# Performance work log

Hardware: AMD Instinct MI355X
Metric: run time of the kernel (lower is better)

Reference implementation:

```python
import jax, jax.numpy as jnp
import numpy as np

B, CLS, C, H, HP, WP, K = 16, 20, 512, 4, 32, 32, 9
G = H * CLS  # grapher channels = 80
EPS = 1e-5
BNS = 1.0 / np.sqrt(1.0 + EPS)  # eval-mode BN, running_mean=0, running_var=1


def _bn(x, g, b, axis):
    shape = [1] * x.ndim
    shape[axis] = -1
    return x * (g * BNS).reshape(shape) + b.reshape(shape)


def setup_inputs():
    key = jax.random.key(0)
    ks = jax.random.split(key, 16)
    def rn(k, shp, scale=0.02):
        return jax.random.normal(k, shp, dtype=jnp.float32) * scale
    return {
        "x_cls": jax.random.normal(ks[0], (B, CLS, C), jnp.float32),
        "x_patch": jax.random.normal(ks[1], (B, C, HP, WP), jnp.float32),
        "norm_x_w": jnp.ones((C, 1, 1), jnp.float32),
        "norm_x_b": jnp.zeros((C, 1, 1), jnp.float32),
        "pq_w": rn(ks[2], (C, C)), "pq_b": rn(ks[3], (C,)),
        "ncls_w": jnp.ones((C,), jnp.float32), "ncls_b": jnp.zeros((C,), jnp.float32),
        "pkv_w": rn(ks[4], (2 * C, C)), "pkv_b": rn(ks[5], (2 * C,)),
        "fc1_w": rn(ks[6], (G, G)), "fc1_b": rn(ks[7], (G,)),
        "bn1_g": jnp.ones((G,), jnp.float32), "bn1_b": jnp.zeros((G,), jnp.float32),
        "mr_w": rn(ks[8], (2 * G, 2 * G // H)), "mr_b": rn(ks[9], (2 * G,)),
        "bn2_g": jnp.ones((2 * G,), jnp.float32), "bn2_b": jnp.zeros((2 * G,), jnp.float32),
        "fc2_w": rn(ks[10], (G, 2 * G)), "fc2_b": rn(ks[11], (G,)),
        "bn3_g": jnp.ones((G,), jnp.float32), "bn3_b": jnp.zeros((G,), jnp.float32),
        "proj_w": rn(ks[12], (C, C)), "proj_b": rn(ks[13], (C,)),
    }


def _forward(x_cls, x_patch, norm_x_w, norm_x_b, pq_w, pq_b, ncls_w, ncls_b,
             pkv_w, pkv_b, fc1_w, fc1_b, bn1_g, bn1_b, mr_w, mr_b, bn2_g, bn2_b,
             fc2_w, fc2_b, bn3_g, bn3_b, proj_w, proj_b):
    hd = C // H
    N = HP * WP
    scale = hd ** -0.5
    # norm_x: LayerNormGeneral over (C,H,W)
    c0 = x_patch - x_patch.mean(axis=(1, 2, 3), keepdims=True)
    s0 = (c0 * c0).mean(axis=(1, 2, 3), keepdims=True)
    xn = c0 / jnp.sqrt(s0 + EPS) * norm_x_w + norm_x_b
    # proj_q (1x1 conv) -> multi-head query [B,H,N,hd]
    q = jnp.einsum('oc,bchw->bohw', pq_w, xn) + pq_b[None, :, None, None]
    q = q.reshape(B, H, hd, N).transpose(0, 1, 3, 2)
    # norm_cls: LayerNorm over channel dim
    m = x_cls.mean(-1, keepdims=True)
    v = ((x_cls - m) ** 2).mean(-1, keepdims=True)
    xc = (x_cls - m) / jnp.sqrt(v + EPS) * ncls_w + ncls_b
    kv = xc @ pkv_w.T + pkv_b                                  # [B,Cls,2C]
    k_, v_ = kv[..., :C], kv[..., C:]
    key_ = k_.reshape(B, CLS, H, hd).transpose(0, 2, 3, 1)     # [B,H,hd,Cls]
    val = v_.reshape(B, CLS, H, hd).transpose(0, 2, 1, 3)      # [B,H,Cls,hd]
    attn = jnp.einsum('bhnd,bhdc->bhnc', q, key_) * scale      # [B,H,N,Cls]
    amap = attn.reshape(B, H, HP, WP, CLS).transpose(0, 1, 4, 2, 3).reshape(B, G, HP, WP)
    # ---- Grapher (ViG gcn_lib): fc1 -> DyGraphConv(MRConv, KNN) -> fc2 -> residual ----
    sc = amap
    x = jnp.einsum('oc,bchw->bohw', fc1_w, amap) + fc1_b[None, :, None, None]
    x = _bn(x, bn1_g, bn1_b, 1)
    xf = x.reshape(B, G, N).transpose(0, 2, 1)                 # [B,N,G]
    # dense KNN on L2-normalized features (indices only, non-diff)
    xu = xf / jnp.maximum(jnp.linalg.norm(xf, axis=-1, keepdims=True), 1e-12)
    sq = jnp.sum(xu * xu, axis=-1)                             # [B,N]
    neg_d = 2.0 * jnp.einsum('bnc,bmc->bnm', xu, xu) - sq[:, :, None] - sq[:, None, :]
    _, nn_idx = jax.lax.top_k(neg_d, K)                        # [B,N,K]
    neigh = xf[jnp.arange(B)[:, None, None], nn_idx]           # [B,N,K,G]
    xj = jnp.max(neigh - xf[:, :, None, :], axis=2)            # [B,N,G] max-relative
    y = jnp.stack([xf, xj], axis=-1).reshape(B, N, 2 * G)      # interleave (x0,xj0,x1,...)
    # grouped 1x1 conv (groups=H), BN, GELU
    yg = y.reshape(B, N, H, 2 * G // H)
    wg = mr_w.reshape(H, 2 * G // H, 2 * G // H)
    z = jnp.einsum('bngi,goi->bngo', yg, wg).reshape(B, N, 2 * G) + mr_b
    z = _bn(z, bn2_g, bn2_b, 2)
    z = jax.nn.gelu(z, approximate=False)
    z2 = z @ fc2_w.T + fc2_b                                   # [B,N,G]
    z2 = _bn(z2, bn3_g, bn3_b, 2)
    gout = z2.transpose(0, 2, 1).reshape(B, G, HP, WP) + sc
    # ---- softmax-weighted value aggregation ----
    attn2 = gout.reshape(B, H, CLS, N).transpose(0, 1, 3, 2)   # [B,H,N,Cls]
    attn2 = jax.nn.softmax(attn2, axis=-1)
    out = jnp.einsum('bhnc,bhcd->bhnd', attn2, val)            # [B,H,N,hd]
    out = out.transpose(0, 1, 3, 2).reshape(B, C, HP, WP)
    out = jnp.einsum('oc,bchw->bohw', proj_w, out) + proj_b[None, :, None, None]
    return x_patch + out


def reference(x_cls, x_patch, norm_x_w, norm_x_b, pq_w, pq_b, ncls_w, ncls_b,
              pkv_w, pkv_b, fc1_w, fc1_b, bn1_g, bn1_b, mr_w, mr_b, bn2_g, bn2_b,
              fc2_w, fc2_b, bn3_g, bn3_b, proj_w, proj_b):
    return _forward(x_cls, x_patch, norm_x_w, norm_x_b, pq_w, pq_b, ncls_w, ncls_b,
                    pkv_w, pkv_b, fc1_w, fc1_b, bn1_g, bn1_b, mr_w, mr_b, bn2_g, bn2_b,
                    fc2_w, fc2_b, bn3_g, bn3_b, proj_w, proj_b)
```

## Files before the change

### kernel.cpp

```cpp
#include <hip/hip_runtime.h>
#include <math.h>

#define DI __device__ __forceinline__

constexpr int B_ = 16, CLS_ = 20, C_ = 512, H_ = 4, HD_ = 128, N_ = 1024, G_ = 80, G2_ = 160, K_ = 9;
constexpr float EPS_ = 1e-5f;
constexpr float BNS_ = 0.9999950000374997f;
constexpr float SCALE_ = 0.08838834764831845f;
constexpr float INVSQRT2_ = 0.7071067811865475f;

typedef __attribute__((ext_vector_type(8))) short bf16x8;
typedef __attribute__((ext_vector_type(4))) float f32x4;

constexpr long OFF_PART  = 0;
constexpr long OFF_STATS = 2048;
constexpr long OFF_EB    = 4096;
constexpr long OFF_EBB   = OFF_EB    + 524288;
constexpr long OFF_KV    = OFF_EBB   + 2048;
constexpr long OFF_AMAPT = OFF_KV    + 327680;
constexpr long OFF_XF    = OFF_AMAPT + 1310720;
constexpr long OFF_XUB   = OFF_XF    + 1310720;
constexpr long OFF_W1BD  = OFF_XUB   + 786432;
constexpr long OFF_FC2B  = OFF_W1BD  + 16384;
constexpr long OFF_SQ    = OFF_FC2B  + 8192;
constexpr long OFF_NEGD  = OFF_SQ    + 16384;
constexpr long OFF_GOUTT = OFF_NEGD  + 16777216 + 147456;
constexpr long OFF_WPB   = OFF_GOUTT + 1310720;
constexpr long OFF_Y     = OFF_WPB   + 131072;
constexpr long OFF_AMAPB = OFF_Y     + 1310720;
constexpr long OFF_FC1B  = OFF_AMAPB + 786432;
constexpr long OFF_PB    = OFF_FC1B  + 4096;

DI float wsum(float v){
#pragma unroll
  for(int d=1; d<64; d<<=1) v += __shfl_xor(v, d);
  return v;
}
DI unsigned short f2b(float f){
  unsigned u = __float_as_uint(f);
  unsigned r = (u + 0x7FFFu + ((u >> 16) & 1u)) >> 16;
  return (unsigned short)r;
}

#define GLOAD16(g, s) __builtin_amdgcn_global_load_lds((const __attribute__((address_space(1))) void*)(g), \
                        (__attribute__((address_space(3))) void*)(s), 16, 0, 0)

__global__ __launch_bounds__(256) void k_stats_partial(const float* __restrict__ x, float* __restrict__ part){
  int blk = blockIdx.x;
  const float4* xp = (const float4*)x;
  long base4 = (long)blk * 2048;
  int t = threadIdx.x;
  float s = 0.f, ss = 0.f;
#pragma unroll
  for(int j=0;j<8;++j){
    float4 v = xp[base4 + t + 256*j];
    s  += v.x + v.y + v.z + v.w;
    ss += v.x*v.x + v.y*v.y + v.z*v.z + v.w*v.w;
  }
  s = wsum(s); ss = wsum(ss);
  __shared__ float rs[4], rss[4];
  int wv = t >> 6;
  if((t & 63) == 0){ rs[wv] = s; rss[wv] = ss; }
  __syncthreads();
  if(t == 0){
    part[blk*2]   = rs[0]+rs[1]+rs[2]+rs[3];
    part[blk*2+1] = rss[0]+rss[1]+rss[2]+rss[3];
  }
}

__global__ __launch_bounds__(64) void k_stats_final(const float* __restrict__ part, float* __restrict__ stats){
  int b = blockIdx.x, t = threadIdx.x;
  float s  = part[(b*64+t)*2];
  float ss = part[(b*64+t)*2+1];
  s = wsum(s); ss = wsum(ss);
  if(t == 0){
    const float cnt = (float)(C_ * N_);
    float m = s / cnt;
    float var = ss / cnt - m*m;
    stats[b*2]   = m;
    stats[b*2+1] = 1.0f / sqrtf(var + EPS_);
  }
}

__global__ __launch_bounds__(256) void k_wprep(const float* __restrict__ projw, unsigned short* __restrict__ wpb,
                                               const float* __restrict__ mrw, const float* __restrict__ fc2w,
                                               const float* __restrict__ fc1w,
                                               unsigned short* __restrict__ w1bd, unsigned short* __restrict__ fc2b16,
                                               unsigned short* __restrict__ fc1b16){
  int blk = blockIdx.x, t = threadIdx.x;
  if(blk < 256){
    long i = (long)blk*256 + t;
    float4 v = ((const float4*)projw)[i];
    uint2 o;
    o.x = (unsigned)f2b(v.x) | ((unsigned)f2b(v.y) << 16);
    o.y = (unsigned)f2b(v.z) | ((unsigned)f2b(v.w) << 16);
    ((uint2*)wpb)[i] = o;
    return;
  }
  int row = blk - 256;
  if(row < 160){
    if(t < 160){
      unsigned short v = 0;
      if(t/40 == row/40) v = f2b(mrw[row*40 + (t % 40)]);
      w1bd[row*160 + t] = v;
    }
  } else if(row < 240){
    if(t < 160) fc2b16[(row-160)*160 + t] = f2b(fc2w[(long)(row-160)*160 + t]);
  } else {
    int r = row - 240;
    if(t < 96) fc1b16[r*96 + t] = (t < G_) ? f2b(fc1w[(long)r*G_ + t]) : (unsigned short)0;
  }
}

__global__ __launch_bounds__(256) void k_eprep(const float* __restrict__ kv, const float* __restrict__ pqw,
                                               const float* __restrict__ pqb, const float* __restrict__ stats,
                                               const float* __restrict__ nw, const float* __restrict__ nbv,
                                               unsigned short* __restrict__ Eb, float* __restrict__ ebb,
                                               float* __restrict__ pb){
  int b = blockIdx.x, hh = blockIdx.y, cch = blockIdx.z, t = threadIdx.x;
  if(hh == 4){
    if(cch == 0){
      unsigned* z = (unsigned*)(Eb + ((long)b*128 + 80)*512);
      for(int i=t; i<12288; i+=256) z[i] = 0;
    }
    return;
  }
  int h = hh, c0 = cch*64;
  float m = stats[b*2], inv = stats[b*2+1];
  __shared__ float key[CLS_][HD_];
  __shared__ float part[4][CLS_][64];
  for(int i=t; i<CLS_*HD_; i+=256){
    int cls = i >> 7, d = i & 127;
    key[cls][d] = kv[((long)b*CLS_+cls)*1024 + h*HD_ + d];
  }
  __syncthreads();
  int c = t & 63, ds = t >> 6;
  float acc[CLS_] = {};
  const float* wp = pqw + ((long)(h*HD_ + ds*32))*C_ + c0 + c;
#pragma unroll 8
  for(int di=0; di<32; ++di){
    float wv = wp[(long)di*C_];
#pragma unroll
    for(int cls=0; cls<CLS_; ++cls) acc[cls] += key[cls][ds*32+di]*wv;
  }
#pragma unroll
  for(int cls=0; cls<CLS_; ++cls) part[ds][cls][c] = acc[cls];
  __syncthreads();
  for(int i=t; i<CLS_*64; i+=256){
    int cls = i >> 6, cc = i & 63;
    float v = (part[0][cls][cc]+part[1][cls][cc]+part[2][cls][cc]+part[3][cls][cc]) * SCALE_;
    int cg = c0 + cc;
    float a = inv * nw[cg];
    float bbv = nbv[cg] - m*a;
    Eb[((long)b*128 + h*CLS_ + cls)*512 + cg] = f2b(v*a);
    part[0][cls][cc] = v*bbv;
  }
  __syncthreads();
  if(t < CLS_){
    float s = 0.f;
    for(int cc=0; cc<64; ++cc) s += part[0][t][cc];
    pb[((long)b*8 + cch)*G_ + h*CLS_ + t] = s;
  }
  if(cch == 0 && t >= 64 && t < 64 + CLS_){
    int tt = t - 64;
    float bacc = 0.f;
    for(int d=0; d<HD_; ++d) bacc += key[tt][d]*pqb[h*HD_+d];
    ebb[b*G_ + h*CLS_ + tt] = bacc*SCALE_;
  }
}

__global__ __launch_bounds__(256) void k_amap_gemm(const unsigned short* __restrict__ Eb,
                                                   const float* __restrict__ xp,
                                                   const float* __restrict__ ebb,
                                                   const float* __restrict__ pb,
                                                   float* __restrict__ amapT,
                                                   unsigned short* __restrict__ amapb){
  __shared__ unsigned short Xl[64*520];
  __shared__ unsigned short Bgl[4096];
  int b = blockIdx.y, n0 = blockIdx.x*64;
  int t = threadIdx.x, w = t >> 6, l = t & 63;
  int wr = w >> 1, wc = w & 1;
  {
    int nb = t & 7, cl = t >> 3;
    const float* xb = xp + (long)b*C_*N_ + n0 + nb*8;
#pragma unroll 4
    for(int pass=0; pass<16; ++pass){
      int c = pass*32 + cl;
      const float* src = xb + (long)c*N_;
      float4 v0 = *(const float4*)src;
      float4 v1 = *(const float4*)(src+4);
      int base = (nb*8)*520 + c;
      Xl[base         ] = f2b(v0.x);
      Xl[base + 520   ] = f2b(v0.y);
      Xl[base + 520*2 ] = f2b(v0.z);
      Xl[base + 520*3 ] = f2b(v0.w);
      Xl[base + 520*4 ] = f2b(v1.x);
      Xl[base + 520*5 ] = f2b(v1.y);
      Xl[base + 520*6 ] = f2b(v1.z);
      Xl[base + 520*7 ] = f2b(v1.w);
    }
  }
  __syncthreads();
  f32x4 acc[2][4] = {};
  const unsigned short* Bt = Eb + ((long)b*128 + w*16 + (l>>2))*512 + (l&3)*8;
  int ra = wr*32 + (l & 15);
  int rb = wc*64 + (l & 15);
  int kq = (l >> 4) * 8;
  for(int k0 = 0; k0 < 512; k0 += 32){
    if(k0) __syncthreads();
    GLOAD16(Bt + k0,          &Bgl[w*512]);
    GLOAD16(Bt + 64*512 + k0, &Bgl[2048 + w*512]);
    __syncthreads();
    bf16x8 af[2], bfr[4];
#pragma unroll
    for(int rt=0; rt<2; ++rt) af[rt]  = *(const bf16x8*)&Xl[(ra + rt*16)*520 + k0 + kq];
#pragma unroll
    for(int ct=0; ct<4; ++ct) bfr[ct] = *(const bf16x8*)&Bgl[(rb + ct*16)*32 + kq];
#pragma unroll
    for(int rt=0; rt<2; ++rt)
#pragma unroll
      for(int ct=0; ct<4; ++ct)
        acc[rt][ct] = __builtin_amdgcn_mfma_f32_16x16x32_bf16(af[rt], bfr[ct], acc[rt][ct], 0, 0, 0);
  }
  float bias4[4];
#pragma unroll
  for(int ct=0; ct<4; ++ct){
    int g = wc*64 + ct*16 + (l & 15);
    float bi = 0.f;
    if(g < G_){
      bi = ebb[b*G_ + g];
#pragma unroll
      for(int cc=0; cc<8; ++cc) bi += pb[((long)b*8 + cc)*G_ + g];
    }
    bias4[ct] = bi;
  }
  int r0 = (l >> 4)*4;
#pragma unroll
  for(int rt=0; rt<2; ++rt){
#pragma unroll
    for(int r=0; r<4; ++r){
      int n = n0 + wr*32 + rt*16 + r0 + r;
      long rowb  = ((long)b*N_ + n)*G_;
      long rowb9 = ((long)b*N_ + n)*96;
#pragma unroll
      for(int ct=0; ct<4; ++ct){
        int g = wc*64 + ct*16 + (l & 15);
        if(g < G_){
          float val = acc[rt][ct][r] + bias4[ct];
          amapT[rowb + g] = val;
          amapb[rowb9 + g] = f2b(val);
        } else if(g < 96){
          amapb[rowb9 + g] = 0;
        }
      }
    }
  }
}

template<bool RES>
__global__ __launch_bounds__(256) void k_gemm_mfma(const unsigned short* __restrict__ Wb,
                                                   const unsigned short* __restrict__ Xb,
                                                   const float* __restrict__ bias,
                                                   const float* __restrict__ Res,
                                                   float* __restrict__ Out){
  __shared__ unsigned short Al[4096];
  __shared__ unsigned short Bl[4096];
  int b = blockIdx.z;
  int o0 = blockIdx.y*128, n0 = blockIdx.x*128;
  int t = threadIdx.x, w = t >> 6, l = t & 63;
  int wr = w >> 1, wc = w & 1;
  f32x4 acc[4][4] = {};
  const unsigned short* Wt = Wb + (long)(o0 + w*16 + (l>>2))*512 + (l&3)*8;
  const unsigned short* Xt = Xb + ((long)b*N_ + n0 + w*16 + (l>>2))*512 + (l&3)*8;
  int ra = wr*64 + (l & 15);
  int rb = wc*64 + (l & 15);
  int kq = (l >> 4) * 8;
  for(int k0 = 0; k0 < 512; k0 += 32){
    if(k0) __syncthreads();
    GLOAD16(Wt + k0,            &Al[w*512]);
    GLOAD16(Wt + 64*512 + k0,   &Al[2048 + w*512]);
    GLOAD16(Xt + k0,            &Bl[w*512]);
    GLOAD16(Xt + 64*512 + k0,   &Bl[2048 + w*512]);
    __syncthreads();
    bf16x8 af[4], bfr[4];
#pragma unroll
    for(int i=0;i<4;++i){
      af[i]  = *(const bf16x8*)&Al[(ra + i*16)*32 + kq];
      bfr[i] = *(const bf16x8*)&Bl[(rb + i*16)*32 + kq];
    }
#pragma unroll
    for(int mi=0; mi<4; ++mi)
#pragma unroll
      for(int ni=0; ni<4; ++ni)
        acc[mi][ni] = __builtin_amdgcn_mfma_f32_16x16x32_bf16(af[mi], bfr[ni], acc[mi][ni], 0, 0, 0);
  }
  long obase = ((long)b*C_ + o0 + wr*64)*N_ + n0 + wc*64 + (l & 15);
  int r0 = (l >> 4) * 4;
#pragma unroll
  for(int mi=0; mi<4; ++mi){
#pragma unroll
    for(int r=0; r<4; ++r){
      int row = mi*16 + r0 + r;
      float bi = bias[o0 + wr*64 + row];
#pragma unroll
      for(int ni=0; ni<4; ++ni){
        long oi = obase + (long)row*N_ + ni*16;
        float v = acc[mi][ni][r] + bi;
        if(RES) v += Res[oi];
        Out[oi] = v;
      }
    }
  }
}

__global__ __launch_bounds__(256) void k_cls_kv(const float* __restrict__ xcls,
                                                const float* __restrict__ ncw, const float* __restrict__ ncb,
                                                const float* __restrict__ pkvw, const float* __restrict__ pkvb,
                                                float* __restrict__ kv){
  int b = blockIdx.x;
  int ochunk = blockIdx.y;
  __shared__ float xc[CLS_][C_];
  int t = threadIdx.x, wv = t >> 6, l = t & 63;
  for(int cls = wv; cls < CLS_; cls += 4){
    const float* xr = xcls + ((long)b*CLS_ + cls) * C_;
    float vals[8];
    float s = 0.f, ss = 0.f;
#pragma unroll
    for(int j=0;j<8;++j){ float v = xr[l + 64*j]; vals[j] = v; s += v; ss += v*v; }
    s = wsum(s); ss = wsum(ss);
    float m = s / (float)C_;
    float var = ss / (float)C_ - m*m;
    float inv = 1.0f / sqrtf(var + EPS_);
#pragma unroll
    for(int j=0;j<8;++j){
      int c = l + 64*j;
      xc[cls][c] = (vals[j]-m)*inv*ncw[c] + ncb[c];
    }
  }
  __syncthreads();
  int o = ochunk*128 + (t & 127);
  int cls0 = (t >> 7) * 10;
  float acc[10] = {};
  const float* wrow = pkvw + (long)o * C_;
  for(int k4 = 0; k4 < C_; k4 += 4){
    float4 w4 = *(const float4*)&wrow[k4];
#pragma unroll
    for(int i=0;i<10;++i){
      acc[i] += w4.x*xc[cls0+i][k4] + w4.y*xc[cls0+i][k4+1] + w4.z*xc[cls0+i][k4+2] + w4.w*xc[cls0+i][k4+3];
    }
  }
  float bo = pkvb[o];
#pragma unroll
  for(int i=0;i<10;++i) kv[((long)b*CLS_ + cls0+i)*1024 + o] = acc[i] + bo;
}

__global__ __launch_bounds__(256) void k_fc1_mfma(const unsigned short* __restrict__ amapb,
                                                  const unsigned short* __restrict__ w1b,
                                                  const float* __restrict__ bias,
                                                  const float* __restrict__ g1, const float* __restrict__ b1,
                                                  float* __restrict__ xf, unsigned short* __restrict__ xub,
                                                  float* __restrict__ sq){
  int t = threadIdx.x, w = t >> 6, l = t & 63;
  long row0 = ((long)blockIdx.x*4 + w)*16;
  int lr = l & 15, lk = l >> 4;
  bf16x8 ay[3];
  const unsigned short* arow = amapb + (row0 + lr)*96 + lk*8;
#pragma unroll
  for(int ks=0; ks<3; ++ks) ay[ks] = *(const bf16x8*)&arow[ks*32];
  f32x4 acc[5] = {};
  const unsigned short* wrow = w1b + (long)lr*96 + lk*8;
#pragma unroll
  for(int ks=0; ks<3; ++ks){
#pragma unroll
    for(int ct=0; ct<5; ++ct){
      bf16x8 bw = *(const bf16x8*)&wrow[ct*16*96 + ks*32];
      acc[ct] = __builtin_amdgcn_mfma_f32_16x16x32_bf16(ay[ks], bw, acc[ct], 0, 0, 0);
    }
  }
  float v[5][4];
  float ssq[4] = {0.f,0.f,0.f,0.f};
#pragma unroll
  for(int ct=0; ct<5; ++ct){
    int o = ct*16 + lr;
    float bi = bias[o], ga = g1[o]*BNS_, bb = b1[o];
#pragma unroll
    for(int i=0;i<4;++i){
      float vv = (acc[ct][i] + bi)*ga + bb;
      v[ct][i] = vv;
      ssq[i] += vv*vv;
    }
  }
#pragma unroll
  for(int d=1; d<16; d<<=1){
#pragma unroll
    for(int i=0;i<4;++i) ssq[i] += __shfl_xor(ssq[i], d);
  }
#pragma unroll
  for(int i=0;i<4;++i){
    long row = row0 + lk*4 + i;
    float invn = 1.0f / fmaxf(sqrtf(ssq[i]), 1e-12f);
#pragma unroll
    for(int ct=0; ct<5; ++ct){
      int o = ct*16 + lr;
      xf[row*G_ + o] = v[ct][i];
      xub[row*96 + o] = f2b(v[ct][i]*invn);
    }
    xub[row*96 + 80 + lr] = 0;
    if(lr == 0) sq[row] = ssq[i]*invn*invn;
  }
}

__global__ __launch_bounds__(256) void k_negd_mfma(const unsigned short* __restrict__ xub,
                                                   const float* __restrict__ sq,
                                                   float* __restrict__ negd){
  __shared__ unsigned short Al[128*96];
  __shared__ unsigned short Bl[128*96];
  int b = blockIdx.z;
  int n0 = blockIdx.y*128, m0 = blockIdx.x*128;
  int t = threadIdx.x, w = t >> 6, l = t & 63;
  int wr = w >> 1, wc = w & 1;
  const unsigned short* gA = xub + ((long)b*N_ + n0)*96;
  const unsigned short* gB = xub + ((long)b*N_ + m0)*96;
#pragma unroll
  for(int rd=0; rd<6; ++rd){
    int chunk = rd*4 + w;
    GLOAD16(gA + chunk*512 + l*8, &Al[chunk*512]);
    GLOAD16(gB + chunk*512 + l*8, &Bl[chunk*512]);
  }
  __syncthreads();
  f32x4 acc[4][4] = {};
  int ra = wr*64 + (l & 15);
  int rb = wc*64 + (l & 15);
#pragma unroll
  for(int ks=0; ks<3; ++ks){
    int kq = ks*32 + (l >> 4)*8;
    bf16x8 af[4], bfr[4];
#pragma unroll
    for(int i=0;i<4;++i){
      af[i]  = *(const bf16x8*)&Al[(ra + i*16)*96 + kq];
      bfr[i] = *(const bf16x8*)&Bl[(rb + i*16)*96 + kq];
    }
#pragma unroll
    for(int mi=0; mi<4; ++mi)
#pragma unroll
      for(int ni=0; ni<4; ++ni)
        acc[mi][ni] = __builtin_amdgcn_mfma_f32_16x16x32_bf16(af[mi], bfr[ni], acc[mi][ni], 0, 0, 0);
  }
  int r0 = (l >> 4)*4;
  const float* sqb = sq + (long)b*N_;
#pragma unroll
  for(int mi=0; mi<4; ++mi){
#pragma unroll
    for(int r=0; r<4; ++r){
      int n = n0 + wr*64 + mi*16 + r0 + r;
      float sn = sqb[n];
      long row = ((long)b*N_ + n)*N_;
#pragma unroll
      for(int ni=0; ni<4; ++ni){
        int m = m0 + wc*64 + ni*16 + (l & 15);
        negd[row + m] = 2.f*acc[mi][ni][r] - sn - sqb[m];
      }
    }
  }
}

__global__ __launch_bounds__(256) void k_topk_y(const float* __restrict__ negd, const float* __restrict__ xf,
                                                unsigned short* __restrict__ y){
  int t = threadIdx.x, wv = t >> 6, l = t & 63;
  long r = (long)blockIdx.x*4 + wv;
  long b = r >> 10;
  const float* row = negd + r*N_;
  float vals[16];
#pragma unroll
  for(int j=0;j<16;++j) vals[j] = row[l + 64*j];
  int nbs[K_];
#pragma unroll
  for(int p=0; p<K_; ++p){
    float bv = vals[0]; int bj = 0;
#pragma unroll
    for(int j=1;j<16;++j) if(vals[j] > bv){ bv = vals[j]; bj = j; }
    int bm = l + 64*bj;
#pragma unroll
    for(int d=1; d<64; d<<=1){
      float ov = __shfl_xor(bv, d);
      int   om = __shfl_xor(bm, d);
      if(ov > bv || (ov == bv && om < bm)){ bv = ov; bm = om; }
    }
    nbs[p] = bm;
#pragma unroll
    for(int j=0;j<16;++j) if(bm == l + 64*j) vals[j] = -INFINITY;
  }
  const float* frow = xf + r*G_;
  int o2s = (l < 16) ? (64 + l) : 0;
  float f0 = frow[l];
  float f1 = frow[o2s];
  float m0 = -INFINITY, m1 = -INFINITY;
#pragma unroll
  for(int k=0;k<K_;++k){
    const float* nr = xf + ((long)b*N_ + nbs[k])*G_;
    m0 = fmaxf(m0, nr[l]);
    m1 = fmaxf(m1, nr[o2s]);
  }
  unsigned short* yr = y + r*G2_;
  ushort2 u0; u0.x = f2b(f0); u0.y = f2b(m0 - f0);
  *(ushort2*)&yr[2*l] = u0;
  if(l < 16){
    ushort2 u1; u1.x = f2b(f1); u1.y = f2b(m1 - f1);
    *(ushort2*)&yr[128 + 2*l] = u1;
  }
}

__global__ __launch_bounds__(256) void k_mixer_mfma(const unsigned short* __restrict__ y,
                                                    const unsigned short* __restrict__ w1bd,
                                                    const float* __restrict__ mrb,
                                                    const float* __restrict__ g2, const float* __restrict__ b2,
                                                    const unsigned short* __restrict__ fc2b16,
                                                    const float* __restrict__ fc2bias,
                                                    const float* __restrict__ g3, const float* __restrict__ b3,
                                                    const float* __restrict__ amapT, float* __restrict__ goutT){
  __shared__ unsigned short zl[4][16][G2_];
  int t = threadIdx.x, w = t >> 6, l = t & 63;
  long row0 = ((long)blockIdx.x*4 + w)*16;
  int lr = l & 15, lk = l >> 4;
  bf16x8 ay[5];
  const unsigned short* yrow = y + (row0 + lr)*G2_ + lk*8;
#pragma unroll
  for(int ks=0; ks<5; ++ks) ay[ks] = *(const bf16x8*)&yrow[ks*32];
  f32x4 accz[10] = {};
  const unsigned short* wb = w1bd + (long)lr*G2_ + lk*8;
#pragma unroll
  for(int ks=0; ks<5; ++ks){
#pragma unroll
    for(int ct=0; ct<10; ++ct){
      bf16x8 bw = *(const bf16x8*)&wb[ct*16*G2_ + ks*32];
      accz[ct] = __builtin_amdgcn_mfma_f32_16x16x32_bf16(ay[ks], bw, accz[ct], 0, 0, 0);
    }
  }
#pragma unroll
  for(int ct=0; ct<10; ++ct){
    int o = ct*16 + lr;
    float bi = mrb[o], ga = g2[o]*BNS_, bb = b2[o];
#pragma unroll
    for(int i=0;i<4;++i){
      float v = (accz[ct][i] + bi)*ga + bb;
      float zz = v * 0.5f * (1.0f + erff(v * INVSQRT2_));
      zl[w][lk*4 + i][o] = f2b(zz);
    }
  }
  __syncthreads();
  bf16x8 az[5];
#pragma unroll
  for(int ks=0; ks<5; ++ks) az[ks] = *(const bf16x8*)&zl[w][lr][ks*32 + lk*8];
  f32x4 acc2[5] = {};
  const unsigned short* fb = fc2b16 + (long)lr*G2_ + lk*8;
#pragma unroll
  for(int ks=0; ks<5; ++ks){
#pragma unroll
    for(int ct=0; ct<5; ++ct){
      bf16x8 bw = *(const bf16x8*)&fb[ct*16*G2_ + ks*32];
      acc2[ct] = __builtin_amdgcn_mfma_f32_16x16x32_bf16(az[ks], bw, acc2[ct], 0, 0, 0);
    }
  }
#pragma unroll
  for(int ct=0; ct<5; ++ct){
    int o = ct*16 + lr;
    float bi = fc2bias[o], ga = g3[o]*BNS_, bb = b3[o];
#pragma unroll
    for(int i=0;i<4;++i){
      long row = row0 + lk*4 + i;
      float v = (acc2[ct][i] + bi)*ga + bb + amapT[row*G_ + o];
      goutT[row*G_ + o] = v;
    }
  }
}

__global__ __launch_bounds__(256) void k_softmax_pv(const float* __restrict__ goutT, const float* __restrict__ kv,
                                                    unsigned short* __restrict__ aob){
  int bh = blockIdx.x; int b = bh >> 2, h = bh & 3;
  int n0 = blockIdx.y * 64;
  __shared__ unsigned short Vt[128*32];
  __shared__ unsigned short Pl[64*40];
  __shared__ unsigned short Os[64*132];
  int t = threadIdx.x, w = t >> 6, l = t & 63;
  if(t < 128){
    int d = t;
    const float* vb = kv + ((long)b*CLS_)*1024 + C_ + h*HD_ + d;
#pragma unroll
    for(int cls=0; cls<CLS_; ++cls) Vt[d*32+cls] = f2b(vb[(long)cls*1024]);
#pragma unroll
    for(int cls=CLS_; cls<32; ++cls) Vt[d*32+cls] = 0;
  }
  if(t < 64){
    int n = n0 + t;
    const float* gr = goutT + ((long)b*N_ + n)*G_ + h*CLS_;
    float x[CLS_];
    float mx = -INFINITY;
#pragma unroll
    for(int cls=0; cls<CLS_; ++cls){ x[cls] = gr[cls]; mx = fmaxf(mx, x[cls]); }
    float s = 0.f;
#pragma unroll
    for(int cls=0; cls<CLS_; ++cls){ x[cls] = expf(x[cls]-mx); s += x[cls]; }
    float inv = 1.0f / s;
#pragma unroll
    for(int cls=0; cls<CLS_; ++cls) Pl[t*40+cls] = f2b(x[cls]*inv);
#pragma unroll
    for(int cls=CLS_; cls<32; ++cls) Pl[t*40+cls] = 0;
  }
  __syncthreads();
  int lr = l & 15, kq = (l >> 4)*8;
  f32x4 acc[4][2] = {};
  bf16x8 af[4], bf2[2];
#pragma unroll
  for(int rt=0; rt<4; ++rt) af[rt] = *(const bf16x8*)&Pl[(rt*16+lr)*40 + kq];
#pragma unroll
  for(int ci=0; ci<2; ++ci) bf2[ci] = *(const bf16x8*)&Vt[((2*w+ci)*16+lr)*32 + kq];
#pragma unroll
  for(int rt=0; rt<4; ++rt)
#pragma unroll
    for(int ci=0; ci<2; ++ci)
      acc[rt][ci] = __builtin_amdgcn_mfma_f32_16x16x32_bf16(af[rt], bf2[ci], acc[rt][ci], 0, 0, 0);
  int r0 = (l >> 4)*4;
#pragma unroll
  for(int rt=0; rt<4; ++rt)
#pragma unroll
    for(int ci=0; ci<2; ++ci)
#pragma unroll
      for(int i=0; i<4; ++i)
        Os[(rt*16 + r0 + i)*132 + (2*w+ci)*16 + lr] = f2b(acc[rt][ci][i]);
  __syncthreads();
  unsigned short* ob = aob + ((long)b*N_ + n0)*C_ + h*HD_;
#pragma unroll
  for(int j=0; j<8; ++j){
    int idx = t + 256*j;
    int row = idx >> 5, ch = idx & 31;
    *(ushort4*)&ob[(long)row*C_ + ch*4] =
        *(const ushort4*)&Os[row*132 + ch*4];
  }
}

extern "C" void kernel_launch(void* const* d_in, const int* in_sizes, int n_in,
                              void* d_out, int out_size, void* d_ws, size_t ws_size,
                              hipStream_t stream){
  const float* x_cls   = (const float*)d_in[0];
  const float* x_patch = (const float*)d_in[1];
  const float* norm_x_w = (const float*)d_in[2];
  const float* norm_x_b = (const float*)d_in[3];
  const float* pq_w  = (const float*)d_in[4];
  const float* pq_b  = (const float*)d_in[5];
  const float* ncls_w = (const float*)d_in[6];
  const float* ncls_b = (const float*)d_in[7];
  const float* pkv_w = (const float*)d_in[8];
  const float* pkv_b = (const float*)d_in[9];
  const float* fc1_w = (const float*)d_in[10];
  const float* fc1_b = (const float*)d_in[11];
  const float* bn1_g = (const float*)d_in[12];
  const float* bn1_b = (const float*)d_in[13];
  const float* mr_w  = (const float*)d_in[14];
  const float* mr_b  = (const float*)d_in[15];
  const float* bn2_g = (const float*)d_in[16];
  const float* bn2_b = (const float*)d_in[17];
  const float* fc2_w = (const float*)d_in[18];
  const float* fc2_b = (const float*)d_in[19];
  const float* bn3_g = (const float*)d_in[20];
  const float* bn3_b = (const float*)d_in[21];
  const float* proj_w = (const float*)d_in[22];
  const float* proj_b = (const float*)d_in[23];

  float* ws = (float*)d_ws;
  float* part   = ws + OFF_PART;
  float* stats  = ws + OFF_STATS;
  float* ebb    = ws + OFF_EBB;
  float* kvbuf  = ws + OFF_KV;
  float* amapT  = ws + OFF_AMAPT;
  float* xf     = ws + OFF_XF;
  float* sqbuf  = ws + OFF_SQ;
  float* negd   = ws + OFF_NEGD;
  float* goutT  = ws + OFF_GOUTT;
  float* pbuf   = ws + OFF_PB;
  unsigned short* Eb     = (unsigned short*)(ws + OFF_EB);
  unsigned short* xub    = (unsigned short*)(ws + OFF_XUB);
  unsigned short* w1bd   = (unsigned short*)(ws + OFF_W1BD);
  unsigned short* fc2b16 = (unsigned short*)(ws + OFF_FC2B);
  unsigned short* ybuf   = (unsigned short*)(ws + OFF_Y);
  unsigned short* amapb  = (unsigned short*)(ws + OFF_AMAPB);
  unsigned short* fc1b16 = (unsigned short*)(ws + OFF_FC1B);
  unsigned short* aob = (unsigned short*)(ws + OFF_NEGD);
  unsigned short* wpb = (unsigned short*)(ws + OFF_WPB);
  float* out = (float*)d_out;

  k_stats_partial<<<1024, 256, 0, stream>>>(x_patch, part);
  k_stats_final<<<16, 64, 0, stream>>>(part, stats);
  k_cls_kv<<<dim3(16,8), 256, 0, stream>>>(x_cls, ncls_w, ncls_b, pkv_w, pkv_b, kvbuf);
  k_eprep<<<dim3(16,5,8), 256, 0, stream>>>(kvbuf, pq_w, pq_b, stats, norm_x_w, norm_x_b, Eb, ebb, pbuf);
  k_wprep<<<576, 256, 0, stream>>>(proj_w, wpb, mr_w, fc2_w, fc1_w, w1bd, fc2b16, fc1b16);
  k_amap_gemm<<<dim3(16,16), 256, 0, stream>>>(Eb, x_patch, ebb, pbuf, amapT, amapb);
  k_fc1_mfma<<<256, 256, 0, stream>>>(amapb, fc1b16, fc1_b, bn1_g, bn1_b, xf, xub, sqbuf);
  k_negd_mfma<<<dim3(8,8,16), 256, 0, stream>>>(xub, sqbuf, negd);
  k_topk_y<<<4096, 256, 0, stream>>>(negd, xf, ybuf);
  k_mixer_mfma<<<256, 256, 0, stream>>>(ybuf, w1bd, mr_b, bn2_g, bn2_b,
                                        fc2b16, fc2_b, bn3_g, bn3_b, amapT, goutT);
  k_softmax_pv<<<dim3(64,16), 256, 0, stream>>>(goutT, kvbuf, aob);
  k_gemm_mfma<true><<<dim3(8,4,16), 256, 0, stream>>>(wpb, aob, proj_b, x_patch, out);
}
```

Baseline: 181.4 us.

## Fuse prep kernels, fold stats finalisation into eprep, fuse fc1 into amap GEMM

Merges the x_patch stats partial reduction, the cls LayerNorm plus kv projection, and the weight bf16 conversion into one k_pre launch that dispatches on block index. The per-batch stats finalisation moves into k_eprep. The fc1 MFMA with BN and L2 normalisation moves into the amap GEMM epilogue, reading the bf16 amap tile from LDS instead of a global amapb buffer. This removes four launches and a global round trip for amapb. In exchange, every k_pre block reserves 40KB of LDS, which may limit occupancy of the stats blocks, and k_eprep repeats the stats reduction in each block.

```diff
diff --git a/kernel.cpp b/kernel.cpp
--- a/kernel.cpp
+++ b/kernel.cpp
@@ -13,7 +13,6 @@
 typedef __attribute__((ext_vector_type(4))) float f32x4;
 
 constexpr long OFF_PART  = 0;
-constexpr long OFF_STATS = 2048;
 constexpr long OFF_EB    = 4096;
 constexpr long OFF_EBB   = OFF_EB    + 524288;
 constexpr long OFF_KV    = OFF_EBB   + 2048;
@@ -27,8 +26,7 @@
 constexpr long OFF_GOUTT = OFF_NEGD  + 16777216 + 147456;
 constexpr long OFF_WPB   = OFF_GOUTT + 1310720;
 constexpr long OFF_Y     = OFF_WPB   + 131072;
-constexpr long OFF_AMAPB = OFF_Y     + 1310720;
-constexpr long OFF_FC1B  = OFF_AMAPB + 786432;
+constexpr long OFF_FC1B  = OFF_Y     + 1310720;
 constexpr long OFF_PB    = OFF_FC1B  + 4096;
 
 DI float wsum(float v){
@@ -45,51 +43,79 @@
 #define GLOAD16(g, s) __builtin_amdgcn_global_load_lds((const __attribute__((address_space(1))) void*)(g), \
                         (__attribute__((address_space(3))) void*)(s), 16, 0, 0)
 
-__global__ __launch_bounds__(256) void k_stats_partial(const float* __restrict__ x, float* __restrict__ part){
-  int blk = blockIdx.x;
-  const float4* xp = (const float4*)x;
-  long base4 = (long)blk * 2048;
-  int t = threadIdx.x;
-  float s = 0.f, ss = 0.f;
-#pragma unroll
-  for(int j=0;j<8;++j){
-    float4 v = xp[base4 + t + 256*j];
-    s  += v.x + v.y + v.z + v.w;
-    ss += v.x*v.x + v.y*v.y + v.z*v.z + v.w*v.w;
-  }
-  s = wsum(s); ss = wsum(ss);
-  __shared__ float rs[4], rss[4];
-  int wv = t >> 6;
-  if((t & 63) == 0){ rs[wv] = s; rss[wv] = ss; }
-  __syncthreads();
-  if(t == 0){
-    part[blk*2]   = rs[0]+rs[1]+rs[2]+rs[3];
-    part[blk*2+1] = rss[0]+rss[1]+rss[2]+rss[3];
-  }
-}
-
-__global__ __launch_bounds__(64) void k_stats_final(const float* __restrict__ part, float* __restrict__ stats){
-  int b = blockIdx.x, t = threadIdx.x;
-  float s  = part[(b*64+t)*2];
-  float ss = part[(b*64+t)*2+1];
-  s = wsum(s); ss = wsum(ss);
-  if(t == 0){
-    const float cnt = (float)(C_ * N_);
-    float m = s / cnt;
-    float var = ss / cnt - m*m;
-    stats[b*2]   = m;
-    stats[b*2+1] = 1.0f / sqrtf(var + EPS_);
-  }
-}
-
-__global__ __launch_bounds__(256) void k_wprep(const float* __restrict__ projw, unsigned short* __restrict__ wpb,
-                                               const float* __restrict__ mrw, const float* __restrict__ fc2w,
-                                               const float* __restrict__ fc1w,
-                                               unsigned short* __restrict__ w1bd, unsigned short* __restrict__ fc2b16,
-                                               unsigned short* __restrict__ fc1b16){
+__global__ __launch_bounds__(256) void k_pre(const float* __restrict__ x, float* __restrict__ part,
+                                             const float* __restrict__ xcls,
+                                             const float* __restrict__ ncw, const float* __restrict__ ncb,
+                                             const float* __restrict__ pkvw, const float* __restrict__ pkvb,
+                                             float* __restrict__ kv,
+                                             const float* __restrict__ projw, unsigned short* __restrict__ wpb,
+                                             const float* __restrict__ mrw, const float* __restrict__ fc2w,
+                                             const float* __restrict__ fc1w,
+                                             unsigned short* __restrict__ w1bd, unsigned short* __restrict__ fc2b16,
+                                             unsigned short* __restrict__ fc1b16){
+  __shared__ float sh[CLS_*C_];
   int blk = blockIdx.x, t = threadIdx.x;
-  if(blk < 256){
-    long i = (long)blk*256 + t;
+  if(blk < 1024){
+    const float4* xp = (const float4*)x;
+    long base4 = (long)blk * 2048;
+    float s = 0.f, ss = 0.f;
+#pragma unroll
+    for(int j=0;j<8;++j){
+      float4 v = xp[base4 + t + 256*j];
+      s  += v.x + v.y + v.z + v.w;
+      ss += v.x*v.x + v.y*v.y + v.z*v.z + v.w*v.w;
+    }
+    s = wsum(s); ss = wsum(ss);
+    int wv = t >> 6;
+    if((t & 63) == 0){ sh[wv] = s; sh[4+wv] = ss; }
+    __syncthreads();
+    if(t == 0){
+      part[blk*2]   = sh[0]+sh[1]+sh[2]+sh[3];
+      part[blk*2+1] = sh[4]+sh[5]+sh[6]+sh[7];
+    }
+    return;
+  }
+  if(blk < 1152){
+    int idx = blk - 1024;
+    int b = idx >> 3, ochunk = idx & 7;
+    float (*xc)[C_] = (float(*)[C_])sh;
+    int wv = t >> 6, l = t & 63;
+    for(int cls = wv; cls < CLS_; cls += 4){
+      const float* xr = xcls + ((long)b*CLS_ + cls) * C_;
+      float vals[8];
+      float s = 0.f, ss = 0.f;
+#pragma unroll
+      for(int j=0;j<8;++j){ float v = xr[l + 64*j]; vals[j] = v; s += v; ss += v*v; }
+      s = wsum(s); ss = wsum(ss);
+      float m = s / (float)C_;
+      float var = ss / (float)C_ - m*m;
+      float inv = 1.0f / sqrtf(var + EPS_);
+#pragma unroll
+      for(int j=0;j<8;++j){
+        int c = l + 64*j;
+        xc[cls][c] = (vals[j]-m)*inv*ncw[c] + ncb[c];
+      }
+    }
+    __syncthreads();
+    int o = ochunk*128 + (t & 127);
+    int cls0 = (t >> 7) * 10;
+    float acc[10] = {};
+    const float* wrow = pkvw + (long)o * C_;
+    for(int k4 = 0; k4 < C_; k4 += 4){
+      float4 w4 = *(const float4*)&wrow[k4];
+#pragma unroll
+      for(int i=0;i<10;++i){
+        acc[i] += w4.x*xc[cls0+i][k4] + w4.y*xc[cls0+i][k4+1] + w4.z*xc[cls0+i][k4+2] + w4.w*xc[cls0+i][k4+3];
+      }
+    }
+    float bo = pkvb[o];
+#pragma unroll
+    for(int i=0;i<10;++i) kv[((long)b*CLS_ + cls0+i)*1024 + o] = acc[i] + bo;
+    return;
+  }
+  int blk2 = blk - 1152;
+  if(blk2 < 256){
+    long i = (long)blk2*256 + t;
     float4 v = ((const float4*)projw)[i];
     uint2 o;
     o.x = (unsigned)f2b(v.x) | ((unsigned)f2b(v.y) << 16);
@@ -97,7 +123,7 @@
     ((uint2*)wpb)[i] = o;
     return;
   }
-  int row = blk - 256;
+  int row = blk2 - 256;
   if(row < 160){
     if(t < 160){
       unsigned short v = 0;
@@ -106,14 +132,14 @@
     }
   } else if(row < 240){
     if(t < 160) fc2b16[(row-160)*160 + t] = f2b(fc2w[(long)(row-160)*160 + t]);
-  } else {
+  } else if(row < 320){
     int r = row - 240;
     if(t < 96) fc1b16[r*96 + t] = (t < G_) ? f2b(fc1w[(long)r*G_ + t]) : (unsigned short)0;
   }
 }
 
 __global__ __launch_bounds__(256) void k_eprep(const float* __restrict__ kv, const float* __restrict__ pqw,
-                                               const float* __restrict__ pqb, const float* __restrict__ stats,
+                                               const float* __restrict__ pqb, const float* __restrict__ partbuf,
                                                const float* __restrict__ nw, const float* __restrict__ nbv,
                                                unsigned short* __restrict__ Eb, float* __restrict__ ebb,
                                                float* __restrict__ pb){
@@ -125,15 +151,27 @@
     }
     return;
   }
-  int h = hh, c0 = cch*64;
-  float m = stats[b*2], inv = stats[b*2+1];
+  __shared__ float sst[2];
   __shared__ float key[CLS_][HD_];
   __shared__ float part[4][CLS_][64];
+  if(t < 64){
+    float s  = partbuf[(b*64+t)*2];
+    float ss = partbuf[(b*64+t)*2+1];
+    s = wsum(s); ss = wsum(ss);
+    if(t == 0){
+      const float cnt = (float)(C_ * N_);
+      float m = s / cnt;
+      sst[0] = m;
+      sst[1] = 1.0f / sqrtf(ss / cnt - m*m + EPS_);
+    }
+  }
+  int h = hh, c0 = cch*64;
   for(int i=t; i<CLS_*HD_; i+=256){
     int cls = i >> 7, d = i & 127;
     key[cls][d] = kv[((long)b*CLS_+cls)*1024 + h*HD_ + d];
   }
   __syncthreads();
+  float m = sst[0], inv = sst[1];
   int c = t & 63, ds = t >> 6;
   float acc[CLS_] = {};
   const float* wp = pqw + ((long)(h*HD_ + ds*32))*C_ + c0 + c;
@@ -159,7 +197,7 @@
   if(t < CLS_){
     float s = 0.f;
     for(int cc=0; cc<64; ++cc) s += part[0][t][cc];
-    pb[((long)b*8 + cch)*G_ + h*CLS_ + t] = s;
+    pb[((long)b*8 + cch)*G_ + t < 0 ? 0 : ((long)b*8 + cch)*G_ + h*CLS_ + t] = s;
   }
   if(cch == 0 && t >= 64 && t < 64 + CLS_){
     int tt = t - 64;
@@ -169,14 +207,19 @@
   }
 }
 
-__global__ __launch_bounds__(256) void k_amap_gemm(const unsigned short* __restrict__ Eb,
-                                                   const float* __restrict__ xp,
-                                                   const float* __restrict__ ebb,
-                                                   const float* __restrict__ pb,
-                                                   float* __restrict__ amapT,
-                                                   unsigned short* __restrict__ amapb){
+__global__ __launch_bounds__(256) void k_amap_fc1(const unsigned short* __restrict__ Eb,
+                                                  const float* __restrict__ xp,
+                                                  const float* __restrict__ ebb,
+                                                  const float* __restrict__ pb,
+                                                  const unsigned short* __restrict__ w1b,
+                                                  const float* __restrict__ f1bias,
+                                                  const float* __restrict__ g1, const float* __restrict__ b1,
+                                                  float* __restrict__ amapT,
+                                                  float* __restrict__ xf, unsigned short* __restrict__ xub,
+                                                  float* __restrict__ sq){
   __shared__ unsigned short Xl[64*520];
   __shared__ unsigned short Bgl[4096];
+  unsigned short* A1 = Xl;
   int b = blockIdx.y, n0 = blockIdx.x*64;
   int t = threadIdx.x, w = t >> 6, l = t & 63;
   int wr = w >> 1, wc = w & 1;
@@ -234,26 +277,74 @@
     }
     bias4[ct] = bi;
   }
+  __syncthreads();
   int r0 = (l >> 4)*4;
 #pragma unroll
   for(int rt=0; rt<2; ++rt){
 #pragma unroll
     for(int r=0; r<4; ++r){
-      int n = n0 + wr*32 + rt*16 + r0 + r;
-      long rowb  = ((long)b*N_ + n)*G_;
-      long rowb9 = ((long)b*N_ + n)*96;
+      int lrow = wr*32 + rt*16 + r0 + r;
+      long rowb = ((long)b*N_ + n0 + lrow)*G_;
 #pragma unroll
       for(int ct=0; ct<4; ++ct){
         int g = wc*64 + ct*16 + (l & 15);
         if(g < G_){
           float val = acc[rt][ct][r] + bias4[ct];
           amapT[rowb + g] = val;
-          amapb[rowb9 + g] = f2b(val);
+          A1[lrow*96 + g] = f2b(val);
         } else if(g < 96){
-          amapb[rowb9 + g] = 0;
+          A1[lrow*96 + g] = 0;
         }
       }
     }
+  }
+  __syncthreads();
+  int lr = l & 15, lk = l >> 4;
+  bf16x8 ay[3];
+  const unsigned short* arow = &A1[(w*16 + lr)*96 + lk*8];
+#pragma unroll
+  for(int ks=0; ks<3; ++ks) ay[ks] = *(const bf16x8*)&arow[ks*32];
+  f32x4 acc5[5] = {};
+  const unsigned short* wrow = w1b + (long)lr*96 + lk*8;
+#pragma unroll
+  for(int ks=0; ks<3; ++ks){
+#pragma unroll
+    for(int ct=0; ct<5; ++ct){
+      bf16x8 bw = *(const bf16x8*)&wrow[ct*16*96 + ks*32];
+      acc5[ct] = __builtin_amdgcn_mfma_f32_16x16x32_bf16(ay[ks], bw, acc5[ct], 0, 0, 0);
+    }
+  }
+  float v[5][4];
+  float ssq[4] = {0.f,0.f,0.f,0.f};
+#pragma unroll
+  for(int ct=0; ct<5; ++ct){
+    int o = ct*16 + lr;
+    float bi = f1bias[o], ga = g1[o]*BNS_, bb = b1[o];
+#pragma unroll
+    for(int i=0;i<4;++i){
+      float vv = (acc5[ct][i] + bi)*ga + bb;
+      v[ct][i] = vv;
+      ssq[i] += vv*vv;
+    }
+  }
+#pragma unroll
+  for(int d=1; d<16; d<<=1){
+#pragma unroll
+    for(int i=0;i<4;++i) ssq[i] += __shfl_xor(ssq[i], d);
+  }
+  long row0g = (long)b*N_ + n0 + w*16;
+#pragma unroll
+  for(int i=0;i<4;++i){
+    long row = row0g + lk*4 + i;
+    float invn = 1.0f / fmaxf(sqrtf(ssq[i]), 1e-12f);
+#pragma unroll
+    for(int ct=0; ct<5; ++ct){
+      int o = ct*16 + lr;
+      xf[row*G_ + o] = v[ct][i];
+      xub[row*96 + o] = f2b(v[ct][i]*invn);
+    }
+    xub[row*96 + 80 + lr] = 0;
+    if(lr == 0) sq[row] = ssq[i]*invn*invn;
   }
 }
 
@@ -310,103 +401,6 @@
         Out[oi] = v;
       }
     }
-  }
-}
-
-__global__ __launch_bounds__(256) void k_cls_kv(const float* __restrict__ xcls,
-                                                const float* __restrict__ ncw, const float* __restrict__ ncb,
-                                                const float* __restrict__ pkvw, const float* __restrict__ pkvb,
-                                                float* __restrict__ kv){
-  int b = blockIdx.x;
-  int ochunk = blockIdx.y;
-  __shared__ float xc[CLS_][C_];
-  int t = threadIdx.x, wv = t >> 6, l = t & 63;
-  for(int cls = wv; cls < CLS_; cls += 4){
-    const float* xr = xcls + ((long)b*CLS_ + cls) * C_;
-    float vals[8];
-    float s = 0.f, ss = 0.f;
-#pragma unroll
-    for(int j=0;j<8;++j){ float v = xr[l + 64*j]; vals[j] = v; s += v; ss += v*v; }
-    s = wsum(s); ss = wsum(ss);
-    float m = s / (float)C_;
-    float var = ss / (float)C_ - m*m;
-    float inv = 1.0f / sqrtf(var + EPS_);
-#pragma unroll
-    for(int j=0;j<8;++j){
-      int c = l + 64*j;
-      xc[cls][c] = (vals[j]-m)*inv*ncw[c] + ncb[c];
-    }
-  }
-  __syncthreads();
-  int o = ochunk*128 + (t & 127);
-  int cls0 = (t >> 7) * 10;
-  float acc[10] = {};
-  const float* wrow = pkvw + (long)o * C_;
-  for(int k4 = 0; k4 < C_; k4 += 4){
-    float4 w4 = *(const float4*)&wrow[k4];
-#pragma unroll
-    for(int i=0;i<10;++i){
-      acc[i] += w4.x*xc[cls0+i][k4] + w4.y*xc[cls0+i][k4+1] + w4.z*xc[cls0+i][k4+2] + w4.w*xc[cls0+i][k4+3];
-    }
-  }
-  float bo = pkvb[o];
-#pragma unroll
-  for(int i=0;i<10;++i) kv[((long)b*CLS_ + cls0+i)*1024 + o] = acc[i] + bo;
-}
-
-__global__ __launch_bounds__(256) void k_fc1_mfma(const unsigned short* __restrict__ amapb,
-                                                  const unsigned short* __restrict__ w1b,
-                                                  const float* __restrict__ bias,
-                                                  const float* __restrict__ g1, const float* __restrict__ b1,
-                                                  float* __restrict__ xf, unsigned short* __restrict__ xub,
-                                                  float* __restrict__ sq){
-  int t = threadIdx.x, w = t >> 6, l = t & 63;
-  long row0 = ((long)blockIdx.x*4 + w)*16;
-  int lr = l & 15, lk = l >> 4;
-  bf16x8 ay[3];
-  const unsigned short* arow = amapb + (row0 + lr)*96 + lk*8;
-#pragma unroll
-  for(int ks=0; ks<3; ++ks) ay[ks] = *(const bf16x8*)&arow[ks*32];
-  f32x4 acc[5] = {};
-  const unsigned short* wrow = w1b + (long)lr*96 + lk*8;
-#pragma unroll
-  for(int ks=0; ks<3; ++ks){
-#pragma unroll
-    for(int ct=0; ct<5; ++ct){
-      bf16x8 bw = *(const bf16x8*)&wrow[ct*16*96 + ks*32];
-      acc[ct] = __builtin_amdgcn_mfma_f32_16x16x32_bf16(ay[ks], bw, acc[ct], 0, 0, 0);
-    }
-  }
-  float v[5][4];
-  float ssq[4] = {0.f,0.f,0.f,0.f};
-#pragma unroll
-  for(int ct=0; ct<5; ++ct){
-    int o = ct*16 + lr;
-    float bi = bias[o], ga = g1[o]*BNS_, bb = b1[o];
-#pragma unroll
-    for(int i=0;i<4;++i){
-      float vv = (acc[ct][i] + bi)*ga + bb;
-      v[ct][i] = vv;
-      ssq[i] += vv*vv;
-    }
-  }
-#pragma unroll
-  for(int d=1; d<16; d<<=1){
-#pragma unroll
-    for(int i=0;i<4;++i) ssq[i] += __shfl_xor(ssq[i], d);
-  }
-#pragma unroll
-  for(int i=0;i<4;++i){
-    long row = row0 + lk*4 + i;
-    float invn = 1.0f / fmaxf(sqrtf(ssq[i]), 1e-12f);
-#pragma unroll
-    for(int ct=0; ct<5; ++ct){
-      int o = ct*16 + lr;
-      xf[row*G_ + o] = v[ct][i];
-      xub[row*96 + o] = f2b(v[ct][i]*invn);
-    }
-    xub[row*96 + 80 + lr] = 0;
-    if(lr == 0) sq[row] = ssq[i]*invn*invn;
   }
 }
 
@@ -668,7 +662,6 @@
 
   float* ws = (float*)d_ws;
   float* part   = ws + OFF_PART;
-  float* stats  = ws + OFF_STATS;
   float* ebb    = ws + OFF_EBB;
   float* kvbuf  = ws + OFF_KV;
   float* amapT  = ws + OFF_AMAPT;
@@ -682,19 +675,16 @@
   unsigned short* w1bd   = (unsigned short*)(ws + OFF_W1BD);
   unsigned short* fc2b16 = (unsigned short*)(ws + OFF_FC2B);
   unsigned short* ybuf   = (unsigned short*)(ws + OFF_Y);
-  unsigned short* amapb  = (unsigned short*)(ws + OFF_AMAPB);
   unsigned short* fc1b16 = (unsigned short*)(ws + OFF_FC1B);
   unsigned short* aob = (unsigned short*)(ws + OFF_NEGD);
   unsigned short* wpb = (unsigned short*)(ws + OFF_WPB);
   float* out = (float*)d_out;
 
-  k_stats_partial<<<1024, 256, 0, stream>>>(x_patch, part);
-  k_stats_final<<<16, 64, 0, stream>>>(part, stats);
-  k_cls_kv<<<dim3(16,8), 256, 0, stream>>>(x_cls, ncls_w, ncls_b, pkv_w, pkv_b, kvbuf);
-  k_eprep<<<dim3(16,5,8), 256, 0, stream>>>(kvbuf, pq_w, pq_b, stats, norm_x_w, norm_x_b, Eb, ebb, pbuf);
-  k_wprep<<<576, 256, 0, stream>>>(proj_w, wpb, mr_w, fc2_w, fc1_w, w1bd, fc2b16, fc1b16);
-  k_amap_gemm<<<dim3(16,16), 256, 0, stream>>>(Eb, x_patch, ebb, pbuf, amapT, amapb);
-  k_fc1_mfma<<<256, 256, 0, stream>>>(amapb, fc1b16, fc1_b, bn1_g, bn1_b, xf, xub, sqbuf);
+  k_pre<<<1728, 256, 0, stream>>>(x_patch, part, x_cls, ncls_w, ncls_b, pkv_w, pkv_b, kvbuf,
+                                  proj_w, wpb, mr_w, fc2_w, fc1_w, w1bd, fc2b16, fc1b16);
+  k_eprep<<<dim3(16,5,8), 256, 0, stream>>>(kvbuf, pq_w, pq_b, part, norm_x_w, norm_x_b, Eb, ebb, pbuf);
+  k_amap_fc1<<<dim3(16,16), 256, 0, stream>>>(Eb, x_patch, ebb, pbuf, fc1b16, fc1_b, bn1_g, bn1_b,
+                                              amapT, xf, xub, sqbuf);
   k_negd_mfma<<<dim3(8,8,16), 256, 0, stream>>>(xub, sqbuf, negd);
   k_topk_y<<<4096, 256, 0, stream>>>(negd, xf, ybuf);
   k_mixer_mfma<<<256, 256, 0, stream>>>(ybuf, w1bd, mr_b, bn2_g, bn2_b,
```

After: 174.3 us. 3.9% less time.
